# Kernel tuning notes

Hardware: AMD Instinct MI355X
Metric: run time of the kernel (lower is better)

Reference implementation:

```python
import jax, jax.numpy as jnp
import numpy as np

B, L, H, E, D = 4, 2048, 8, 64, 64  # seq S == L (causal mask requires square scores)


def setup_inputs() -> dict:
    key = jax.random.key(0)
    k0, k1, k2, k3, k4 = jax.random.split(key, 5)
    queries = jax.random.normal(k0, (B, L, H, E), jnp.float32)
    keys = jax.random.normal(k1, (B, L, H, E), jnp.float32)
    values = jax.random.normal(k2, (B, L, H, D), jnp.float32)
    # per-sample learned de-stationary scale (positive) and bias
    tau = jax.random.uniform(k3, (B, 1, 1), jnp.float32, 0.5, 1.5)
    delta = jax.random.normal(k4, (B, 1, L), jnp.float32) * 0.1
    return {"queries": queries, "keys": keys, "values": values, "tau": tau, "delta": delta}


def reference(queries, keys, values, tau, delta):
    Bq, Lq, Hq, Eq = queries.shape
    S = keys.shape[1]
    scale = 1.0 / jnp.sqrt(jnp.asarray(Eq, jnp.float32))
    # torch path: rearrange('b s h d l -> (b d) s h l') with s=h=d=1 -> [B,1,1,1] / [B,1,1,S]
    tau_b = tau.reshape(Bq, 1, 1, 1)
    delta_b = delta.reshape(Bq, 1, 1, -1)[..., :S]
    # scores: [B, H, L, S]
    scores = jnp.einsum('blhe,bshe->bhls', queries, keys) * tau_b + delta_b
    causal = jnp.triu(jnp.ones((Lq, S), bool), k=1)  # True above diagonal -> masked
    scores = jnp.where(causal, -jnp.inf, scores)
    A = jax.nn.softmax(scale * scores, axis=-1)  # dropout is identity in eval/reference
    V = jnp.einsum('bhls,bshd->blhd', A, values)  # [B, L, H, D]
    return V
```

## Files before the change

### kernel.cpp

```cpp
#include <hip/hip_runtime.h>
#include <hip/hip_bf16.h>

#define Bsz 4
#define Lsz 2048
#define Hsz 8
#define Esz 64
#define Dsz 64

typedef __attribute__((ext_vector_type(8))) short bf16x8;
typedef __attribute__((ext_vector_type(4))) float f32x4;

__device__ __forceinline__ short f2bs(float f) {
    union { float f; unsigned u; } v; v.f = f;
    unsigned r = v.u + 0x7FFFu + ((v.u >> 16) & 1u);
    return (short)(r >> 16);
}
__device__ __forceinline__ short f2bs_rh(float f) {
    return (short)((__float_as_uint(f) + 0x8000u) >> 16);
}

template<int CTRL>
__device__ __forceinline__ float dpp_mov_f(float x) {
    return __int_as_float(__builtin_amdgcn_update_dpp(
        0, __float_as_int(x), CTRL, 0xF, 0xF, true));
}
__device__ __forceinline__ float row_sum16(float x) {
    x += dpp_mov_f<0xB1>(x);
    x += dpp_mov_f<0x4E>(x);
    x += dpp_mov_f<0x141>(x);
    x += dpp_mov_f<0x140>(x);
    return x;
}

__device__ __forceinline__ void stage16(const short* g, short* l) {
    __builtin_amdgcn_global_load_lds(
        (const __attribute__((address_space(1))) unsigned int*)g,
        (__attribute__((address_space(3))) unsigned int*)l,
        16, 0, 0);
}

__global__ __launch_bounds__(256) void prep_kv(
    const float* __restrict__ ksrc, const float* __restrict__ vsrc,
    short* __restrict__ Kf, short* __restrict__ Vf)
{
    __shared__ float Vl[64][65];
    const int raw = blockIdx.x;
    const int tid = threadIdx.x;
    if (raw < Bsz*Hsz*32) {
        const int bid = raw;
        const int tl = bid & 31, bh = bid >> 5;
        const int b = bh >> 3, h = bh & 7;
        const int nt = tid >> 6, rest = tid & 63, ln = rest >> 2, quad = rest & 3;
        const int row = tl*64 + nt*16 + ln;
        const float* sp = ksrc + (((size_t)b*Lsz + row)*Hsz + h)*Esz + quad*8;
        float4 a0 = *(const float4*)(sp);
        float4 a1 = *(const float4*)(sp + 4);
        float4 b0 = *(const float4*)(sp + 32);
        float4 b1 = *(const float4*)(sp + 36);
        short* dp = Kf + ((size_t)bid*512 + nt*128 + ln*4 + quad)*8;
        *(bf16x8*)dp = (bf16x8){f2bs(a0.x),f2bs(a0.y),f2bs(a0.z),f2bs(a0.w),
                                f2bs(a1.x),f2bs(a1.y),f2bs(a1.z),f2bs(a1.w)};
        *(bf16x8*)(dp + 512) = (bf16x8){f2bs(b0.x),f2bs(b0.y),f2bs(b0.z),f2bs(b0.w),
                                        f2bs(b1.x),f2bs(b1.y),f2bs(b1.z),f2bs(b1.w)};
    } else {
        const int bid = raw - Bsz*Hsz*32;
        const int tl = bid & 31, bh = bid >> 5;
        const int b = bh >> 3, h = bh & 7;
        const int row = tid >> 2, c0 = (tid & 3) * 16;
        const float* sp = vsrc + (((size_t)b*Lsz + tl*64 + row)*Hsz + h)*Dsz + c0;
        *(float4*)&Vl[row][c0]      = *(const float4*)(sp);
        *(float4*)&Vl[row][c0 + 4]  = *(const float4*)(sp + 4);
        *(float4*)&Vl[row][c0 + 8]  = *(const float4*)(sp + 8);
        *(float4*)&Vl[row][c0 + 12] = *(const float4*)(sp + 12);
        __syncthreads();
        #pragma unroll
        for (int u = 0; u < 2; ++u) {
            const int f = tid*2 + u;
            const int nt = f >> 7, sh = (f >> 6) & 1, ln = (f >> 2) & 15, quad = f & 3;
            const int d = nt*16 + ln, s0 = sh*32 + quad*8;
            bf16x8 p = {f2bs(Vl[s0+0][d]), f2bs(Vl[s0+1][d]),
                        f2bs(Vl[s0+2][d]), f2bs(Vl[s0+3][d]),
                        f2bs(Vl[s0+4][d]), f2bs(Vl[s0+5][d]),
                        f2bs(Vl[s0+6][d]), f2bs(Vl[s0+7][d])};
            *(bf16x8*)(Vf + ((size_t)bid*512 + f)*8) = p;
        }
    }
}

__global__ __launch_bounds__(512, 4) void dsattn_main(
    const float* __restrict__ q,
    const short* __restrict__ Kf,
    const short* __restrict__ Vf,
    const float* __restrict__ tau,
    const float* __restrict__ delta,
    float* __restrict__ out)
{
    __shared__ __align__(16) short Kb[2][4096];
    __shared__ __align__(16) short Vb[2][4096];
    __shared__ float dls[Lsz];
    __shared__ __align__(16) short Ps[8][16][72];

    const int tid  = threadIdx.x;
    const int wv   = tid >> 6;
    const int lane = tid & 63;
    const int ln   = lane & 15;
    const int quad = lane >> 4;

    const int bh = blockIdx.x;
    const int b  = bh >> 3, h = bh & 7;
    const int j  = blockIdx.y;
    const int qt = (j < 8) ? j : 23 - j;
    const int q0 = qt * 128;
    const int T  = 2*qt + 2;

    const float c2  = 0.125f * 1.44269504f;
    const float st2 = c2 * tau[b];

    const short* kt = Kf + (size_t)bh * (32*4096);
    const short* vt = Vf + (size_t)bh * (32*4096);

    {
        const float* dsrc = delta + (size_t)b * Lsz + tid*4;
        float4 a = *(const float4*)(dsrc);
        a.x*=c2; a.y*=c2; a.z*=c2; a.w*=c2;
        *(float4*)&dls[tid*4] = a;
    }

    #pragma unroll
    for (int u = 0; u < 2; ++u) {
        const int c = wv*2 + u;
        const short* g = ((c < 8) ? kt : vt) + (c & 7)*512 + lane*8;
        short* l = ((c < 8) ? &Kb[0][0] : &Vb[0][0]) + (c & 7)*512;
        stage16(g, l);
    }

    bf16x8 qf0, qf1;
    {
        const float* qrow = q + (((size_t)b*Lsz + q0 + wv*16 + ln)*Hsz + h)*Esz;
        float4 a0 = *(const float4*)(qrow + quad*8);
        float4 a1 = *(const float4*)(qrow + quad*8 + 4);
        float4 b0 = *(const float4*)(qrow + 32 + quad*8);
        float4 b1 = *(const float4*)(qrow + 32 + quad*8 + 4);
        qf0 = (bf16x8){f2bs(a0.x),f2bs(a0.y),f2bs(a0.z),f2bs(a0.w),
                       f2bs(a1.x),f2bs(a1.y),f2bs(a1.z),f2bs(a1.w)};
        qf1 = (bf16x8){f2bs(b0.x),f2bs(b0.y),f2bs(b0.z),f2bs(b0.w),
                       f2bs(b1.x),f2bs(b1.y),f2bs(b1.z),f2bs(b1.w)};
    }

    float l_i[4] = {0.f,0.f,0.f,0.f};
    f32x4 oacc[4];
    #pragma unroll
    for (int nt=0;nt<4;nt++) oacc[nt] = (f32x4){0.f,0.f,0.f,0.f};

    const int fo = (ln*4 + quad)*8;
    const int qg = q0 + wv*16;

    __syncthreads();

    for (int t = 0; t < T; ++t) {
        const int cur = t & 1;
        if (t + 1 < T) {
            const int nb = cur ^ 1;
            #pragma unroll
            for (int u = 0; u < 2; ++u) {
                const int c = wv*2 + u;
                const short* g = ((c < 8) ? kt : vt) + (size_t)(t+1)*4096 + (c & 7)*512 + lane*8;
                short* l = ((c < 8) ? &Kb[nb][0] : &Vb[nb][0]) + (c & 7)*512;
                stage16(g, l);
            }
        }

        const short* Kc = &Kb[cur][0];
        const short* Vc = &Vb[cur][0];

        f32x4 sacc[4];
        #pragma unroll
        for (int nt=0;nt<4;nt++){
            bf16x8 kf0 = *(const bf16x8*)(Kc + nt*1024 + fo);
            bf16x8 kf1 = *(const bf16x8*)(Kc + nt*1024 + 512 + fo);
            f32x4 z = (f32x4){0.f,0.f,0.f,0.f};
            z = __builtin_amdgcn_mfma_f32_16x16x32_bf16(qf0, kf0, z, 0,0,0);
            sacc[nt] = __builtin_amdgcn_mfma_f32_16x16x32_bf16(qf1, kf1, z, 0,0,0);
        }

        const int k0 = t * 64;
        float dl[4];
        #pragma unroll
        for (int nt=0;nt<4;nt++) dl[nt] = dls[k0 + nt*16 + ln];

        if (k0 + 63 > qg) {
            #pragma unroll
            for (int nt=0;nt<4;nt++){
                const int key = k0 + nt*16 + ln;
                #pragma unroll
                for (int r=0;r<4;r++){
                    if (key > qg + quad*4 + r) sacc[nt][r] = -1e30f;
                }
            }
        }

        #pragma unroll
        for (int nt=0;nt<4;nt++)
            #pragma unroll
            for (int r=0;r<4;r++){
                float p = __builtin_amdgcn_exp2f(fmaf(sacc[nt][r], st2, dl[nt]));
                l_i[r] += p;
                Ps[wv][quad*4+r][nt*16+ln] = f2bs_rh(p);
            }
        bf16x8 pf0 = *(const bf16x8*)&Ps[wv][ln][quad*8];
        bf16x8 pf1 = *(const bf16x8*)&Ps[wv][ln][32 + quad*8];

        #pragma unroll
        for (int nt=0;nt<4;nt++){
            bf16x8 vf0 = *(const bf16x8*)(Vc + nt*1024 + fo);
            bf16x8 vf1 = *(const bf16x8*)(Vc + nt*1024 + 512 + fo);
            oacc[nt] = __builtin_amdgcn_mfma_f32_16x16x32_bf16(pf0, vf0, oacc[nt], 0,0,0);
            oacc[nt] = __builtin_amdgcn_mfma_f32_16x16x32_bf16(pf1, vf1, oacc[nt], 0,0,0);
        }

        __syncthreads();
    }

    #pragma unroll
    for (int r=0;r<4;r++){
        const float inv = 1.0f / row_sum16(l_i[r]);
        const int qr = qg + quad*4 + r;
        float* orow = out + (((size_t)b*Lsz + qr)*Hsz + h)*Dsz;
        #pragma unroll
        for (int nt=0;nt<4;nt++)
            orow[nt*16+ln] = oacc[nt][r] * inv;
    }
}

extern "C" void kernel_launch(void* const* d_in, const int* in_sizes, int n_in,
                              void* d_out, int out_size, void* d_ws, size_t ws_size,
                              hipStream_t stream) {
    (void)in_sizes; (void)n_in; (void)out_size; (void)ws_size;
    const float* q     = (const float*)d_in[0];
    const float* k     = (const float*)d_in[1];
    const float* v     = (const float*)d_in[2];
    const float* tau   = (const float*)d_in[3];
    const float* delta = (const float*)d_in[4];
    float* out = (float*)d_out;

    short* Kf = (short*)d_ws;
    short* Vf = (short*)d_ws + (size_t)(4*1024*1024);

    prep_kv<<<dim3(Bsz*Hsz*32*2), dim3(256), 0, stream>>>(k, v, Kf, Vf);
    dsattn_main<<<dim3(Bsz*Hsz, 16), dim3(512), 0, stream>>>(q, Kf, Vf, tau, delta, out);
}
```

Measured before the change: 133.9 us.

## Compute transposed S^T tiles so P stays in registers and skip LDS round-trip

The score MFMA is swapped to K*Q^T, so each lane holds probabilities in the layout needed as the B operand of a 16x16x16 MFMA for P*V. This removes the per-tile LDS write and read of P. Each wave now handles 32 query rows with 256 threads per block, which reuses every K/V fragment across two row groups. Waves whose rows end before the last key tile skip it. The K/V prep kernel is reworked to the new fragment layouts, and outputs are written as float4. The cost is higher register pressure, more staging per thread, and fewer waves per block.

```diff
diff --git a/kernel.cpp b/kernel.cpp
--- a/kernel.cpp
+++ b/kernel.cpp
@@ -4,10 +4,9 @@
 #define Bsz 4
 #define Lsz 2048
 #define Hsz 8
-#define Esz 64
-#define Dsz 64
 
 typedef __attribute__((ext_vector_type(8))) short bf16x8;
+typedef __attribute__((ext_vector_type(4))) short bf16x4;
 typedef __attribute__((ext_vector_type(4))) float f32x4;
 
 __device__ __forceinline__ short f2bs(float f) {
@@ -17,19 +16,6 @@
 }
 __device__ __forceinline__ short f2bs_rh(float f) {
     return (short)((__float_as_uint(f) + 0x8000u) >> 16);
-}
-
-template<int CTRL>
-__device__ __forceinline__ float dpp_mov_f(float x) {
-    return __int_as_float(__builtin_amdgcn_update_dpp(
-        0, __float_as_int(x), CTRL, 0xF, 0xF, true));
-}
-__device__ __forceinline__ float row_sum16(float x) {
-    x += dpp_mov_f<0xB1>(x);
-    x += dpp_mov_f<0x4E>(x);
-    x += dpp_mov_f<0x141>(x);
-    x += dpp_mov_f<0x140>(x);
-    return x;
 }
 
 __device__ __forceinline__ void stage16(const short* g, short* l) {
@@ -43,51 +29,53 @@
     const float* __restrict__ ksrc, const float* __restrict__ vsrc,
     short* __restrict__ Kf, short* __restrict__ Vf)
 {
-    __shared__ float Vl[64][65];
+    __shared__ float Tl[64][65];
     const int raw = blockIdx.x;
     const int tid = threadIdx.x;
-    if (raw < Bsz*Hsz*32) {
-        const int bid = raw;
-        const int tl = bid & 31, bh = bid >> 5;
-        const int b = bh >> 3, h = bh & 7;
-        const int nt = tid >> 6, rest = tid & 63, ln = rest >> 2, quad = rest & 3;
-        const int row = tl*64 + nt*16 + ln;
-        const float* sp = ksrc + (((size_t)b*Lsz + row)*Hsz + h)*Esz + quad*8;
-        float4 a0 = *(const float4*)(sp);
-        float4 a1 = *(const float4*)(sp + 4);
-        float4 b0 = *(const float4*)(sp + 32);
-        float4 b1 = *(const float4*)(sp + 36);
-        short* dp = Kf + ((size_t)bid*512 + nt*128 + ln*4 + quad)*8;
-        *(bf16x8*)dp = (bf16x8){f2bs(a0.x),f2bs(a0.y),f2bs(a0.z),f2bs(a0.w),
-                                f2bs(a1.x),f2bs(a1.y),f2bs(a1.z),f2bs(a1.w)};
-        *(bf16x8*)(dp + 512) = (bf16x8){f2bs(b0.x),f2bs(b0.y),f2bs(b0.z),f2bs(b0.w),
-                                        f2bs(b1.x),f2bs(b1.y),f2bs(b1.z),f2bs(b1.w)};
+    const bool isK = raw < Bsz*Hsz*32;
+    const int bid = isK ? raw : raw - Bsz*Hsz*32;
+    const int tl = bid & 31, bh = bid >> 5;
+    const int b = bh >> 3, h = bh & 7;
+
+    const int row = tid >> 2, c0 = (tid & 3) * 16;
+    const float* src = (isK ? ksrc : vsrc)
+                     + (((size_t)b*Lsz + tl*64 + row)*Hsz + h)*64 + c0;
+    *(float4*)&Tl[row][c0]      = *(const float4*)(src);
+    *(float4*)&Tl[row][c0 + 4]  = *(const float4*)(src + 4);
+    *(float4*)&Tl[row][c0 + 8]  = *(const float4*)(src + 8);
+    *(float4*)&Tl[row][c0 + 12] = *(const float4*)(src + 12);
+    __syncthreads();
+
+    const int lane = tid & 63, ln = lane & 15, quad = lane >> 4;
+    if (isK) {
+        short* dst = Kf + (size_t)bid * 4096;
+        #pragma unroll
+        for (int cc = 0; cc < 2; ++cc) {
+            const int c  = (tid >> 6)*2 + cc;
+            const int nt = c >> 1, eh = c & 1;
+            const float* rp = &Tl[nt*16 + ln][eh*32 + quad*8];
+            bf16x8 o = {f2bs(rp[0]),f2bs(rp[1]),f2bs(rp[2]),f2bs(rp[3]),
+                        f2bs(rp[4]),f2bs(rp[5]),f2bs(rp[6]),f2bs(rp[7])};
+            *(bf16x8*)(dst + c*512 + lane*8) = o;
+        }
     } else {
-        const int bid = raw - Bsz*Hsz*32;
-        const int tl = bid & 31, bh = bid >> 5;
-        const int b = bh >> 3, h = bh & 7;
-        const int row = tid >> 2, c0 = (tid & 3) * 16;
-        const float* sp = vsrc + (((size_t)b*Lsz + tl*64 + row)*Hsz + h)*Dsz + c0;
-        *(float4*)&Vl[row][c0]      = *(const float4*)(sp);
-        *(float4*)&Vl[row][c0 + 4]  = *(const float4*)(sp + 4);
-        *(float4*)&Vl[row][c0 + 8]  = *(const float4*)(sp + 8);
-        *(float4*)&Vl[row][c0 + 12] = *(const float4*)(sp + 12);
-        __syncthreads();
-        #pragma unroll
-        for (int u = 0; u < 2; ++u) {
-            const int f = tid*2 + u;
-            const int nt = f >> 7, sh = (f >> 6) & 1, ln = (f >> 2) & 15, quad = f & 3;
-            const int d = nt*16 + ln, s0 = sh*32 + quad*8;
-            bf16x8 p = {f2bs(Vl[s0+0][d]), f2bs(Vl[s0+1][d]),
-                        f2bs(Vl[s0+2][d]), f2bs(Vl[s0+3][d]),
-                        f2bs(Vl[s0+4][d]), f2bs(Vl[s0+5][d]),
-                        f2bs(Vl[s0+6][d]), f2bs(Vl[s0+7][d])};
-            *(bf16x8*)(Vf + ((size_t)bid*512 + f)*8) = p;
-        }
-    }
-}
-
-__global__ __launch_bounds__(512, 4) void dsattn_main(
+        short* dst = Vf + (size_t)bid * 4096;
+        #pragma unroll
+        for (int cc = 0; cc < 2; ++cc) {
+            const int cp  = (tid >> 6)*2 + cc;
+            const int m16 = cp >> 1, nt0 = (cp & 1)*2;
+            const int d   = m16*16 + ln;
+            const int s0  = nt0*16 + quad*4;
+            bf16x8 o = {f2bs(Tl[s0+0][d]),  f2bs(Tl[s0+1][d]),
+                        f2bs(Tl[s0+2][d]),  f2bs(Tl[s0+3][d]),
+                        f2bs(Tl[s0+16][d]), f2bs(Tl[s0+17][d]),
+                        f2bs(Tl[s0+18][d]), f2bs(Tl[s0+19][d])};
+            *(bf16x8*)(dst + cp*512 + lane*8) = o;
+        }
+    }
+}
+
+__global__ __launch_bounds__(256, 2) void dsattn_main(
     const float* __restrict__ q,
     const short* __restrict__ Kf,
     const short* __restrict__ Vf,
@@ -98,7 +86,6 @@
     __shared__ __align__(16) short Kb[2][4096];
     __shared__ __align__(16) short Vb[2][4096];
     __shared__ float dls[Lsz];
-    __shared__ __align__(16) short Ps[8][16][72];
 
     const int tid  = threadIdx.x;
     const int wv   = tid >> 6;
@@ -112,6 +99,7 @@
     const int qt = (j < 8) ? j : 23 - j;
     const int q0 = qt * 128;
     const int T  = 2*qt + 2;
+    const int Tw = (wv < 2) ? T - 1 : T;
 
     const float c2  = 0.125f * 1.44269504f;
     const float st2 = c2 * tau[b];
@@ -120,40 +108,43 @@
     const short* vt = Vf + (size_t)bh * (32*4096);
 
     {
-        const float* dsrc = delta + (size_t)b * Lsz + tid*4;
+        const float* dsrc = delta + (size_t)b*Lsz + tid*8;
         float4 a = *(const float4*)(dsrc);
+        float4 c = *(const float4*)(dsrc + 4);
         a.x*=c2; a.y*=c2; a.z*=c2; a.w*=c2;
-        *(float4*)&dls[tid*4] = a;
-    }
-
-    #pragma unroll
-    for (int u = 0; u < 2; ++u) {
-        const int c = wv*2 + u;
+        c.x*=c2; c.y*=c2; c.z*=c2; c.w*=c2;
+        *(float4*)&dls[tid*8]     = a;
+        *(float4*)&dls[tid*8 + 4] = c;
+    }
+
+    #pragma unroll
+    for (int u = 0; u < 4; ++u) {
+        const int c = wv*4 + u;
         const short* g = ((c < 8) ? kt : vt) + (c & 7)*512 + lane*8;
         short* l = ((c < 8) ? &Kb[0][0] : &Vb[0][0]) + (c & 7)*512;
         stage16(g, l);
     }
 
-    bf16x8 qf0, qf1;
-    {
-        const float* qrow = q + (((size_t)b*Lsz + q0 + wv*16 + ln)*Hsz + h)*Esz;
+    bf16x8 qf[2][2];
+    #pragma unroll
+    for (int hh = 0; hh < 2; ++hh) {
+        const float* qrow = q + (((size_t)b*Lsz + q0 + wv*32 + hh*16 + ln)*Hsz + h)*64;
         float4 a0 = *(const float4*)(qrow + quad*8);
         float4 a1 = *(const float4*)(qrow + quad*8 + 4);
         float4 b0 = *(const float4*)(qrow + 32 + quad*8);
         float4 b1 = *(const float4*)(qrow + 32 + quad*8 + 4);
-        qf0 = (bf16x8){f2bs(a0.x),f2bs(a0.y),f2bs(a0.z),f2bs(a0.w),
-                       f2bs(a1.x),f2bs(a1.y),f2bs(a1.z),f2bs(a1.w)};
-        qf1 = (bf16x8){f2bs(b0.x),f2bs(b0.y),f2bs(b0.z),f2bs(b0.w),
-                       f2bs(b1.x),f2bs(b1.y),f2bs(b1.z),f2bs(b1.w)};
-    }
-
-    float l_i[4] = {0.f,0.f,0.f,0.f};
-    f32x4 oacc[4];
-    #pragma unroll
-    for (int nt=0;nt<4;nt++) oacc[nt] = (f32x4){0.f,0.f,0.f,0.f};
-
-    const int fo = (ln*4 + quad)*8;
-    const int qg = q0 + wv*16;
+        qf[hh][0] = (bf16x8){f2bs(a0.x),f2bs(a0.y),f2bs(a0.z),f2bs(a0.w),
+                             f2bs(a1.x),f2bs(a1.y),f2bs(a1.z),f2bs(a1.w)};
+        qf[hh][1] = (bf16x8){f2bs(b0.x),f2bs(b0.y),f2bs(b0.z),f2bs(b0.w),
+                             f2bs(b1.x),f2bs(b1.y),f2bs(b1.z),f2bs(b1.w)};
+    }
+
+    f32x4 oacc[2][4];
+    #pragma unroll
+    for (int hh = 0; hh < 2; ++hh)
+        #pragma unroll
+        for (int m = 0; m < 4; ++m) oacc[hh][m] = (f32x4){0.f,0.f,0.f,0.f};
+    float l_acc[2] = {0.f, 0.f};
 
     __syncthreads();
 
@@ -162,73 +153,95 @@
         if (t + 1 < T) {
             const int nb = cur ^ 1;
             #pragma unroll
-            for (int u = 0; u < 2; ++u) {
-                const int c = wv*2 + u;
-                const short* g = ((c < 8) ? kt : vt) + (size_t)(t+1)*4096 + (c & 7)*512 + lane*8;
+            for (int u = 0; u < 4; ++u) {
+                const int c = wv*4 + u;
+                const short* g = ((c < 8) ? kt : vt)
+                               + (size_t)(t+1)*4096 + (c & 7)*512 + lane*8;
                 short* l = ((c < 8) ? &Kb[nb][0] : &Vb[nb][0]) + (c & 7)*512;
                 stage16(g, l);
             }
         }
 
-        const short* Kc = &Kb[cur][0];
-        const short* Vc = &Vb[cur][0];
-
-        f32x4 sacc[4];
-        #pragma unroll
-        for (int nt=0;nt<4;nt++){
-            bf16x8 kf0 = *(const bf16x8*)(Kc + nt*1024 + fo);
-            bf16x8 kf1 = *(const bf16x8*)(Kc + nt*1024 + 512 + fo);
-            f32x4 z = (f32x4){0.f,0.f,0.f,0.f};
-            z = __builtin_amdgcn_mfma_f32_16x16x32_bf16(qf0, kf0, z, 0,0,0);
-            sacc[nt] = __builtin_amdgcn_mfma_f32_16x16x32_bf16(qf1, kf1, z, 0,0,0);
-        }
-
-        const int k0 = t * 64;
-        float dl[4];
-        #pragma unroll
-        for (int nt=0;nt<4;nt++) dl[nt] = dls[k0 + nt*16 + ln];
-
-        if (k0 + 63 > qg) {
-            #pragma unroll
-            for (int nt=0;nt<4;nt++){
-                const int key = k0 + nt*16 + ln;
+        if (t < Tw) {
+            const short* Kc = &Kb[cur][0];
+            const short* Vc = &Vb[cur][0];
+            const int k0 = t*64;
+
+            f32x4 sacc[2][4];
+            #pragma unroll
+            for (int nt = 0; nt < 4; ++nt) {
+                bf16x8 kf0 = *(const bf16x8*)(Kc + (nt*2+0)*512 + lane*8);
+                bf16x8 kf1 = *(const bf16x8*)(Kc + (nt*2+1)*512 + lane*8);
                 #pragma unroll
-                for (int r=0;r<4;r++){
-                    if (key > qg + quad*4 + r) sacc[nt][r] = -1e30f;
+                for (int hh = 0; hh < 2; ++hh) {
+                    f32x4 z = (f32x4){0.f,0.f,0.f,0.f};
+                    z = __builtin_amdgcn_mfma_f32_16x16x32_bf16(kf0, qf[hh][0], z, 0,0,0);
+                    sacc[hh][nt] = __builtin_amdgcn_mfma_f32_16x16x32_bf16(kf1, qf[hh][1], z, 0,0,0);
                 }
             }
-        }
-
-        #pragma unroll
-        for (int nt=0;nt<4;nt++)
-            #pragma unroll
-            for (int r=0;r<4;r++){
-                float p = __builtin_amdgcn_exp2f(fmaf(sacc[nt][r], st2, dl[nt]));
-                l_i[r] += p;
-                Ps[wv][quad*4+r][nt*16+ln] = f2bs_rh(p);
+
+            f32x4 dlv[4];
+            #pragma unroll
+            for (int nt = 0; nt < 4; ++nt)
+                dlv[nt] = *(const f32x4*)&dls[k0 + nt*16 + quad*4];
+
+            bf16x4 pT[2][4];
+            #pragma unroll
+            for (int hh = 0; hh < 2; ++hh) {
+                const int qmin = q0 + wv*32 + hh*16;
+                if (k0 + 63 > qmin) {
+                    const int qrow = qmin + ln;
+                    #pragma unroll
+                    for (int nt = 0; nt < 4; ++nt)
+                        #pragma unroll
+                        for (int r = 0; r < 4; ++r)
+                            if (k0 + nt*16 + quad*4 + r > qrow) sacc[hh][nt][r] = -1e30f;
+                }
+                #pragma unroll
+                for (int nt = 0; nt < 4; ++nt) {
+                    float p0 = __builtin_amdgcn_exp2f(fmaf(sacc[hh][nt][0], st2, dlv[nt][0]));
+                    float p1 = __builtin_amdgcn_exp2f(fmaf(sacc[hh][nt][1], st2, dlv[nt][1]));
+                    float p2 = __builtin_amdgcn_exp2f(fmaf(sacc[hh][nt][2], st2, dlv[nt][2]));
+                    float p3 = __builtin_amdgcn_exp2f(fmaf(sacc[hh][nt][3], st2, dlv[nt][3]));
+                    l_acc[hh] += (p0 + p1) + (p2 + p3);
+                    pT[hh][nt] = (bf16x4){f2bs_rh(p0), f2bs_rh(p1), f2bs_rh(p2), f2bs_rh(p3)};
+                }
             }
-        bf16x8 pf0 = *(const bf16x8*)&Ps[wv][ln][quad*8];
-        bf16x8 pf1 = *(const bf16x8*)&Ps[wv][ln][32 + quad*8];
-
-        #pragma unroll
-        for (int nt=0;nt<4;nt++){
-            bf16x8 vf0 = *(const bf16x8*)(Vc + nt*1024 + fo);
-            bf16x8 vf1 = *(const bf16x8*)(Vc + nt*1024 + 512 + fo);
-            oacc[nt] = __builtin_amdgcn_mfma_f32_16x16x32_bf16(pf0, vf0, oacc[nt], 0,0,0);
-            oacc[nt] = __builtin_amdgcn_mfma_f32_16x16x32_bf16(pf1, vf1, oacc[nt], 0,0,0);
+
+            #pragma unroll
+            for (int ntp = 0; ntp < 2; ++ntp)
+                #pragma unroll
+                for (int m16 = 0; m16 < 4; ++m16) {
+                    bf16x8 vv = *(const bf16x8*)(Vc + (m16*2+ntp)*512 + lane*8);
+                    bf16x4 v0 = (bf16x4){vv[0], vv[1], vv[2], vv[3]};
+                    bf16x4 v1 = (bf16x4){vv[4], vv[5], vv[6], vv[7]};
+                    #pragma unroll
+                    for (int hh = 0; hh < 2; ++hh) {
+                        oacc[hh][m16] = __builtin_amdgcn_mfma_f32_16x16x16bf16_1k(
+                            v0, pT[hh][2*ntp+0], oacc[hh][m16], 0,0,0);
+                        oacc[hh][m16] = __builtin_amdgcn_mfma_f32_16x16x16bf16_1k(
+                            v1, pT[hh][2*ntp+1], oacc[hh][m16], 0,0,0);
+                    }
+                }
         }
 
         __syncthreads();
     }
 
     #pragma unroll
-    for (int r=0;r<4;r++){
-        const float inv = 1.0f / row_sum16(l_i[r]);
-        const int qr = qg + quad*4 + r;
-        float* orow = out + (((size_t)b*Lsz + qr)*Hsz + h)*Dsz;
-        #pragma unroll
-        for (int nt=0;nt<4;nt++)
-            orow[nt*16+ln] = oacc[nt][r] * inv;
+    for (int hh = 0; hh < 2; ++hh) {
+        float lsum = l_acc[hh];
+        lsum += __shfl_xor(lsum, 16, 64);
+        lsum += __shfl_xor(lsum, 32, 64);
+        const float inv = 1.0f / lsum;
+        const int qrow = q0 + wv*32 + hh*16 + ln;
+        float* orow = out + (((size_t)b*Lsz + qrow)*Hsz + h)*64;
+        #pragma unroll
+        for (int m16 = 0; m16 < 4; ++m16) {
+            float4 o = {oacc[hh][m16][0]*inv, oacc[hh][m16][1]*inv,
+                        oacc[hh][m16][2]*inv, oacc[hh][m16][3]*inv};
+            *(float4*)(orow + m16*16 + quad*4) = o;
+        }
     }
 }
 
@@ -247,5 +260,5 @@
     short* Vf = (short*)d_ws + (size_t)(4*1024*1024);
 
     prep_kv<<<dim3(Bsz*Hsz*32*2), dim3(256), 0, stream>>>(k, v, Kf, Vf);
-    dsattn_main<<<dim3(Bsz*Hsz, 16), dim3(512), 0, stream>>>(q, Kf, Vf, tau, delta, out);
-}
+    dsattn_main<<<dim3(Bsz*Hsz, 16), dim3(256), 0, stream>>>(q, Kf, Vf, tau, delta, out);
+}
```

Result: no change. 134.8 us (+0.7%).
